# Kernel optimization log

Hardware: AMD Instinct MI355X
Metric: run time of the kernel (lower is better)

## Reference

```python
import jax, jax.numpy as jnp
import numpy as np

D_MODEL = 512
N_HEAD = 8


def setup_inputs() -> dict:
    key = jax.random.key(0)
    ks = jax.random.split(key, 9)
    s = 1.0 / np.sqrt(D_MODEL)
    inp = {
        "x": jax.random.normal(ks[0], (2, 4096, D_MODEL), dtype=jnp.float32),
        "wq": jax.random.uniform(ks[1], (D_MODEL, D_MODEL), jnp.float32, -s, s),
        "bq": jax.random.uniform(ks[2], (D_MODEL,), jnp.float32, -s, s),
        "wk": jax.random.uniform(ks[3], (D_MODEL, D_MODEL), jnp.float32, -s, s),
        "bk": jax.random.uniform(ks[4], (D_MODEL,), jnp.float32, -s, s),
        "wv": jax.random.uniform(ks[5], (D_MODEL, D_MODEL), jnp.float32, -s, s),
        "bv": jax.random.uniform(ks[6], (D_MODEL,), jnp.float32, -s, s),
        "wo": jax.random.uniform(ks[7], (D_MODEL, D_MODEL), jnp.float32, -s, s),
        "bo": jax.random.uniform(ks[8], (D_MODEL,), jnp.float32, -s, s),
    }
    return inp


def reference(x, wq, bq, wk, bk, wv, bv, wo, bo):
    B, S, D = x.shape
    H = N_HEAD
    Dh = D // H

    def split_heads(t):  # [B,S,D] -> [B,H,S,Dh]
        return t.reshape(B, S, H, Dh).transpose(0, 2, 1, 3)

    q = split_heads(x @ wq.T + bq)
    k = split_heads(x @ wk.T + bk)
    v = split_heads(x @ wv.T + bv)

    # explicit (unfused) attention, matching the torch module
    score = jnp.einsum("bhsd,bhtd->bhst", q, k) / jnp.sqrt(jnp.float32(Dh))
    attn = jax.nn.softmax(score, axis=-1)
    out = jnp.einsum("bhst,bhtd->bhsd", attn, v)  # [B,H,S,Dh]

    out = out.transpose(0, 2, 1, 3).reshape(B, S, D)
    return out @ wo.T + bo
```

## Files before the change

### kernel.cpp

```cpp
#include <hip/hip_runtime.h>
#include <math.h>

#define S_LEN 4096
#define DMODEL 512
#define NHEAD 8
#define E_ELEMS ((size_t)8192 * 512)
#define QSCALE 0.18033688f

typedef __attribute__((ext_vector_type(8))) short bf16x8;
typedef __attribute__((ext_vector_type(4))) float f32x4;
typedef __attribute__((ext_vector_type(16))) float f32x16;
typedef unsigned short u16;
typedef unsigned int u32;

__device__ __forceinline__ u16 f2bf(float f) {
    u32 u = __float_as_uint(f);
    u += 0x7FFFu + ((u >> 16) & 1u);
    return (u16)(u >> 16);
}
__device__ __forceinline__ float bf2f(u16 h) {
    return __uint_as_float((u32)h << 16);
}

#define MFMA16(a, b, c) __builtin_amdgcn_mfma_f32_16x16x32_bf16((a), (b), (c), 0, 0, 0)
#define MFMA32(a, b, c) __builtin_amdgcn_mfma_f32_32x32x16_bf16((a), (b), (c), 0, 0, 0)

__global__ __launch_bounds__(256) void cvt_all(
    const float* __restrict__ x,
    const float* __restrict__ wq, const float* __restrict__ wk,
    const float* __restrict__ wv, const float* __restrict__ wo,
    u16* __restrict__ xbf, u16* __restrict__ oq, u16* __restrict__ ok,
    u16* __restrict__ ov, u16* __restrict__ oo)
{
    const int bid = blockIdx.x;
    if (bid < 4096) {
        const int i = bid * 256 + threadIdx.x;
        const float4 v = ((const float4*)x)[i];
        uint2 hp;
        hp.x = (u32)f2bf(v.x) | ((u32)f2bf(v.y) << 16);
        hp.y = (u32)f2bf(v.z) | ((u32)f2bf(v.w) << 16);
        ((uint2*)xbf)[i] = hp;
    } else {
        const int i = (bid - 4096) * 256 + threadIdx.x;
        {
            const float4 v = ((const float4*)wq)[i];
            uint2 hp;
            hp.x = (u32)f2bf(v.x * QSCALE) | ((u32)f2bf(v.y * QSCALE) << 16);
            hp.y = (u32)f2bf(v.z * QSCALE) | ((u32)f2bf(v.w * QSCALE) << 16);
            ((uint2*)oq)[i] = hp;
        }
        {
            const float4 v = ((const float4*)wk)[i];
            uint2 hp;
            hp.x = (u32)f2bf(v.x) | ((u32)f2bf(v.y) << 16);
            hp.y = (u32)f2bf(v.z) | ((u32)f2bf(v.w) << 16);
            ((uint2*)ok)[i] = hp;
        }
        {
            const float4 v = ((const float4*)wv)[i];
            uint2 hp;
            hp.x = (u32)f2bf(v.x) | ((u32)f2bf(v.y) << 16);
            hp.y = (u32)f2bf(v.z) | ((u32)f2bf(v.w) << 16);
            ((uint2*)ov)[i] = hp;
        }
        {
            const float4 v = ((const float4*)wo)[i];
            uint2 hp;
            hp.x = (u32)f2bf(v.x) | ((u32)f2bf(v.y) << 16);
            hp.y = (u32)f2bf(v.z) | ((u32)f2bf(v.w) << 16);
            ((uint2*)oo)[i] = hp;
        }
    }
}

template<int MODE>
__global__ __launch_bounds__(256) void proj2_kernel(
    const u16* __restrict__ Abf,
    const u16* __restrict__ W0, const float* __restrict__ Bi0,
    const u16* __restrict__ W1, const float* __restrict__ Bi1,
    const u16* __restrict__ W2, const float* __restrict__ Bi2,
    u16* __restrict__ Qo, u16* __restrict__ Ko, u16* __restrict__ Vt,
    float* __restrict__ Out)
{
    __shared__ __align__(16) u16 sm[18432];
    u16* As = sm;
    u16* Bs = sm + 8192;

    const int tid = threadIdx.x;
    const int w = tid >> 6, l = tid & 63, g = (l >> 4), c = l & 15;
    const int wr = w >> 1, wc = w & 1;
    const int bm = blockIdx.x * 128;
    const int n0 = blockIdx.y * 128;
    const int z = (MODE == 0) ? blockIdx.z : 0;
    const u16* W   = (z == 0) ? W0 : (z == 1) ? W1 : W2;
    const float* Bi = (z == 0) ? Bi0 : (z == 1) ? Bi1 : Bi2;
    const float bsc = (MODE == 0 && z == 0) ? QSCALE : 1.0f;

    const int sr = l >> 3;
    const int slot = l & 7;

    f32x4 acc[4][4];
    #pragma unroll
    for (int i = 0; i < 4; ++i)
        #pragma unroll
        for (int j = 0; j < 4; ++j) acc[i][j] = (f32x4){0.f, 0.f, 0.f, 0.f};

    #pragma unroll 1
    for (int kt = 0; kt < 8; ++kt) {
        const int k0 = kt * 64;
        __syncthreads();
        #pragma unroll
        for (int i = 0; i < 4; ++i) {
            const int row = i * 32 + w * 8 + sr;
            const int scol = (slot ^ (row & 7)) * 8;
            __builtin_amdgcn_global_load_lds(
                Abf + (size_t)(bm + row) * DMODEL + k0 + scol,
                As + (i * 32 + w * 8) * 64, 16, 0, 0);
            __builtin_amdgcn_global_load_lds(
                W + (size_t)(n0 + row) * DMODEL + k0 + scol,
                Bs + (i * 32 + w * 8) * 64, 16, 0, 0);
        }
        __syncthreads();

        #pragma unroll
        for (int kc = 0; kc < 2; ++kc) {
            bf16x8 a[4], b[4];
            #pragma unroll
            for (int mf = 0; mf < 4; ++mf) {
                const int ra = wr * 64 + mf * 16 + c;
                a[mf] = *(const bf16x8*)(As + ra * 64 + (((kc * 4 + g) ^ (ra & 7)) * 8));
            }
            #pragma unroll
            for (int nf = 0; nf < 4; ++nf) {
                const int rb = wc * 64 + nf * 16 + c;
                b[nf] = *(const bf16x8*)(Bs + rb * 64 + (((kc * 4 + g) ^ (rb & 7)) * 8));
            }
            #pragma unroll
            for (int mf = 0; mf < 4; ++mf)
                #pragma unroll
                for (int nf = 0; nf < 4; ++nf)
                    acc[mf][nf] = MFMA16(a[mf], b[nf], acc[mf][nf]);
        }
    }

    if (MODE == 0 && z == 2) {
        __syncthreads();
        float* scr = (float*)sm;
        const int d = tid & 63, sb = tid >> 6;
        const int b = bm >> 12;
        #pragma unroll
        for (int pass = 0; pass < 2; ++pass) {
            if (wc == pass) {
                #pragma unroll
                for (int mf = 0; mf < 4; ++mf)
                    #pragma unroll
                    for (int nf = 0; nf < 4; ++nf) {
                        const float bias = Bi[n0 + pass * 64 + nf * 16 + c];
                        #pragma unroll
                        for (int r = 0; r < 4; ++r)
                            scr[(wr * 64 + mf * 16 + 4 * g + r) * 72 + nf * 16 + c] =
                                acc[mf][nf][r] + bias;
                    }
            }
            __syncthreads();
            const int hh = (n0 >> 6) + pass;
            const size_t obase =
                ((size_t)((b * NHEAD + hh) * 64 + d)) * S_LEN + (bm & (S_LEN - 1)) + sb * 32;
            u16 th[32];
            #pragma unroll
            for (int j = 0; j < 32; ++j)
                th[j] = f2bf(scr[(sb * 32 + j) * 72 + d]);
            #pragma unroll
            for (int q4 = 0; q4 < 4; ++q4)
                *(uint4*)(Vt + obase + q4 * 8) = *(const uint4*)&th[q4 * 8];
            __syncthreads();
        }
        return;
    }

    #pragma unroll
    for (int mf = 0; mf < 4; ++mf)
        #pragma unroll
        for (int nf = 0; nf < 4; ++nf) {
            const int n = n0 + wc * 64 + nf * 16 + c;
            const float bias = Bi[n] * bsc;
            #pragma unroll
            for (int r = 0; r < 4; ++r) {
                const int m = bm + wr * 64 + mf * 16 + 4 * g + r;
                const float v = acc[mf][nf][r] + bias;
                if (MODE == 1) {
                    Out[(size_t)m * DMODEL + n] = v;
                } else {
                    const int b = m >> 12, s = m & (S_LEN - 1);
                    const int hh = n >> 6, dd = n & 63;
                    const size_t o = ((size_t)((b * NHEAD + hh) * S_LEN + s)) * 64 + dd;
                    if (z == 0) Qo[o] = f2bf(v);
                    else        Ko[o] = f2bf(v);
                }
            }
        }
}

__global__ __launch_bounds__(256, 2) void attn_kernel(
    const u16* __restrict__ Qb, const u16* __restrict__ Kb,
    const u16* __restrict__ Vt, u16* __restrict__ OpB, float* __restrict__ Lp)
{
    __shared__ __align__(16) u16 sm[24576];

    const int tid = threadIdx.x;
    const int w = tid >> 6, l = tid & 63;
    const int r0 = l & 31, hi = l >> 5;

    const int f = blockIdx.x;
    const int wg = (f & 7) * 64 + (f >> 3);
    const int bh = wg >> 5, kvh = (wg >> 4) & 1, qb = wg & 15;
    const int b = bh >> 3, h = bh & 7;

    const size_t hoff = (size_t)bh * S_LEN * 64;
    const int qw = qb * 256 + w * 64;
    const int kv0 = kvh * 2048;

    bf16x8 qf[2][4];
    #pragma unroll
    for (int qfi = 0; qfi < 2; ++qfi)
        #pragma unroll
        for (int kc = 0; kc < 4; ++kc)
            qf[qfi][kc] = *(const bf16x8*)(Qb + hoff +
                (size_t)(qw + qfi * 32 + r0) * 64 + kc * 16 + hi * 8);

    const int rbase = r0 * 64;
    int soff[4];
    #pragma unroll
    for (int j = 0; j < 4; ++j) soff[j] = ((2 * j + hi) ^ (r0 & 7)) * 8;

    const int srow0 = w * 16 + (l >> 3);
    const int slot  = l & 7;
    const int srow1 = srow0 + 8;
    const u16* srcK0 = Kb + hoff + (size_t)(kv0 + srow0) * 64 + ((slot ^ (srow0 & 7)) * 8);
    const u16* srcK1 = Kb + hoff + (size_t)(kv0 + srow1) * 64 + ((slot ^ (srow1 & 7)) * 8);
    const u16* srcV0 = Vt + ((size_t)bh * 64 + srow0) * S_LEN + kv0 + ((slot ^ (srow0 & 7)) * 8);
    const u16* srcV1 = Vt + ((size_t)bh * 64 + srow1) * S_LEN + kv0 + ((slot ^ (srow1 & 7)) * 8);

#define STAGE(bufb, t) do {                                                        \
        u16* kb_ = sm + (bufb) * 8192 + w * 1024;                                  \
        u16* vb_ = kb_ + 4096;                                                     \
        __builtin_amdgcn_global_load_lds(srcK0 + (size_t)(t) * 4096, kb_,       16, 0, 0); \
        __builtin_amdgcn_global_load_lds(srcK1 + (size_t)(t) * 4096, kb_ + 512, 16, 0, 0); \
        __builtin_amdgcn_global_load_lds(srcV0 + (size_t)(t) * 64,   vb_,       16, 0, 0); \
        __builtin_amdgcn_global_load_lds(srcV1 + (size_t)(t) * 64,   vb_ + 512, 16, 0, 0); \
    } while (0)

#define ZERO16 {0.f,0.f,0.f,0.f,0.f,0.f,0.f,0.f,0.f,0.f,0.f,0.f,0.f,0.f,0.f,0.f}
    f32x16 o00 = ZERO16, o01 = ZERO16, o10 = ZERO16, o11 = ZERO16;
    float lA = 0.f, lB = 0.f;

    auto compute_tile = [&](const u16* Kb_s, const u16* Vb_s) {
        #pragma unroll
        for (int kvf = 0; kvf < 2; ++kvf) {
            f32x16 sA = ZERO16, sB = ZERO16;
            __builtin_amdgcn_s_setprio(1);
            #pragma unroll
            for (int kc = 0; kc < 4; ++kc) {
                const bf16x8 k = *(const bf16x8*)(Kb_s + kvf * 2048 + rbase + soff[kc]);
                sA = MFMA32(k, qf[0][kc], sA);
                sB = MFMA32(k, qf[1][kc], sB);
            }
            __builtin_amdgcn_s_setprio(0);

            #pragma unroll
            for (int r = 0; r < 16; ++r) {
                sA[r] = __builtin_amdgcn_exp2f(sA[r]);
                sB[r] = __builtin_amdgcn_exp2f(sB[r]);
            }
            #pragma unroll
            for (int r = 0; r < 16; ++r) { lA += sA[r]; lB += sB[r]; }

            #pragma unroll
            for (int hf = 0; hf < 2; ++hf) {
                const int rb = hf * 8;
                const int idx = kvf * 2 + hf;
                u32 x0, y0, x1, y1;
                asm("v_cvt_pk_bf16_f32 %0, %1, %2" : "=v"(x0) : "v"(sA[rb+0]), "v"(sA[rb+1]));
                asm("v_cvt_pk_bf16_f32 %0, %1, %2" : "=v"(y0) : "v"(sA[rb+4]), "v"(sA[rb+5]));
                asm("v_cvt_pk_bf16_f32 %0, %1, %2" : "=v"(x1) : "v"(sA[rb+2]), "v"(sA[rb+3]));
                asm("v_cvt_pk_bf16_f32 %0, %1, %2" : "=v"(y1) : "v"(sA[rb+6]), "v"(sA[rb+7]));
                asm volatile("v_permlane32_swap_b32 %0, %1" : "+v"(x0), "+v"(y0));
                asm volatile("v_permlane32_swap_b32 %0, %1" : "+v"(x1), "+v"(y1));
                union { u32 u[4]; bf16x8 v; } PA;
                PA.u[0] = x0; PA.u[1] = x1; PA.u[2] = y0; PA.u[3] = y1;
                asm("v_cvt_pk_bf16_f32 %0, %1, %2" : "=v"(x0) : "v"(sB[rb+0]), "v"(sB[rb+1]));
                asm("v_cvt_pk_bf16_f32 %0, %1, %2" : "=v"(y0) : "v"(sB[rb+4]), "v"(sB[rb+5]));
                asm("v_cvt_pk_bf16_f32 %0, %1, %2" : "=v"(x1) : "v"(sB[rb+2]), "v"(sB[rb+3]));
                asm("v_cvt_pk_bf16_f32 %0, %1, %2" : "=v"(y1) : "v"(sB[rb+6]), "v"(sB[rb+7]));
                asm volatile("v_permlane32_swap_b32 %0, %1" : "+v"(x0), "+v"(y0));
                asm volatile("v_permlane32_swap_b32 %0, %1" : "+v"(x1), "+v"(y1));
                union { u32 u[4]; bf16x8 v; } PB;
                PB.u[0] = x0; PB.u[1] = x1; PB.u[2] = y0; PB.u[3] = y1;

                const bf16x8 v0 = *(const bf16x8*)(Vb_s + rbase + soff[idx]);
                const bf16x8 v1 = *(const bf16x8*)(Vb_s + 2048 + rbase + soff[idx]);
                __builtin_amdgcn_s_setprio(1);
                o00 = MFMA32(PA.v, v0, o00);
                o01 = MFMA32(PA.v, v1, o01);
                o10 = MFMA32(PB.v, v0, o10);
                o11 = MFMA32(PB.v, v1, o11);
                __builtin_amdgcn_s_setprio(0);
            }
        }
    };

    STAGE(0, 0);
    STAGE(1, 1);

    #pragma unroll 1
    for (int t = 0; t < 31; ++t) {
        asm volatile("s_waitcnt vmcnt(4)" ::: "memory");
        __builtin_amdgcn_s_barrier();
        __builtin_amdgcn_sched_barrier(0);
        if (t < 30) STAGE((t + 2) % 3, t + 2);
        const u16* Kb_s = sm + (t % 3) * 8192;
        compute_tile(Kb_s, Kb_s + 4096);
    }
    {
        asm volatile("s_waitcnt vmcnt(0)" ::: "memory");
        __builtin_amdgcn_s_barrier();
        __builtin_amdgcn_sched_barrier(0);
        const u16* Kb_s = sm + (31 % 3) * 8192;
        compute_tile(Kb_s, Kb_s + 4096);
    }
#undef STAGE

    lA += __shfl_xor(lA, 32);
    lB += __shfl_xor(lB, 32);
    if (hi == 0) {
        Lp[((size_t)kvh * 16 + bh) * S_LEN + qw + r0]      = lA;
        Lp[((size_t)kvh * 16 + bh) * S_LEN + qw + 32 + r0] = lB;
    }

    u16* Ob = OpB + (size_t)kvh * E_ELEMS + (size_t)b * S_LEN * DMODEL;
    #pragma unroll
    for (int qfi = 0; qfi < 2; ++qfi)
        #pragma unroll
        for (int df = 0; df < 2; ++df) {
            #pragma unroll
            for (int r = 0; r < 16; ++r) {
                const float ov = qfi ? (df ? o11[r] : o10[r]) : (df ? o01[r] : o00[r]);
                const int q = qfi * 32 + (r & 3) + 8 * (r >> 2) + 4 * hi;
                Ob[(size_t)(qw + q) * DMODEL + h * 64 + df * 32 + r0] = f2bf(ov);
            }
        }
}

__global__ __launch_bounds__(256) void combine_kernel(
    const u16* __restrict__ Op, const float* __restrict__ Lp,
    u16* __restrict__ A)
{
    const int i = blockIdx.x * 256 + threadIdx.x;
    const int m = i >> 6;
    const int col = (i & 63) * 8;
    const int b = m >> 12, s = m & (S_LEN - 1), h = col >> 6;
    const int bh = b * 8 + h;

    const float lt = Lp[(size_t)bh * S_LEN + s] +
                     Lp[((size_t)16 + bh) * S_LEN + s];
    const float inv = 1.0f / lt;

    float acc[8] = {};
    #pragma unroll
    for (int kq = 0; kq < 2; ++kq) {
        const uint4 v = *(const uint4*)(Op + (size_t)kq * E_ELEMS + (size_t)m * DMODEL + col);
        const u16* p = (const u16*)&v;
        #pragma unroll
        for (int j = 0; j < 8; ++j) acc[j] += bf2f(p[j]);
    }
    u16 r[8];
    #pragma unroll
    for (int j = 0; j < 8; ++j) r[j] = f2bf(acc[j] * inv);
    *(uint4*)(A + (size_t)m * DMODEL + col) = *(const uint4*)r;
}

extern "C" void kernel_launch(void* const* d_in, const int* in_sizes, int n_in,
                              void* d_out, int out_size, void* d_ws, size_t ws_size,
                              hipStream_t stream)
{
    const float* x  = (const float*)d_in[0];
    const float* wq = (const float*)d_in[1];
    const float* bq = (const float*)d_in[2];
    const float* wk = (const float*)d_in[3];
    const float* bk = (const float*)d_in[4];
    const float* wv = (const float*)d_in[5];
    const float* bv = (const float*)d_in[6];
    const float* wo = (const float*)d_in[7];
    const float* bo = (const float*)d_in[8];

    u16* ws = (u16*)d_ws;
    const size_t E = E_ELEMS;
    u16* xbf  = ws;
    u16* Qbf  = ws + E;
    u16* Kbf  = ws + 2 * E;
    u16* Vtbf = ws + 3 * E;
    u16* wqbf = ws + 4 * E;
    u16* wkbf = wqbf + DMODEL * DMODEL;
    u16* wvbf = wkbf + DMODEL * DMODEL;
    u16* wobf = wvbf + DMODEL * DMODEL;
    u16* OpB  = wobf + DMODEL * DMODEL;
    float* Lp = (float*)(OpB + 2 * E);

    cvt_all<<<dim3(4352), 256, 0, stream>>>(
        x, wq, wk, wv, wo, xbf, wqbf, wkbf, wvbf, wobf);

    proj2_kernel<0><<<dim3(64, 4, 3), 256, 0, stream>>>(
        xbf, wqbf, bq, wkbf, bk, wvbf, bv, Qbf, Kbf, Vtbf, nullptr);

    attn_kernel<<<dim3(512), 256, 0, stream>>>(Qbf, Kbf, Vtbf, OpB, Lp);

    combine_kernel<<<dim3(2048), 256, 0, stream>>>(OpB, Lp, xbf);

    proj2_kernel<1><<<dim3(64, 4, 1), 256, 0, stream>>>(
        xbf, wobf, bo, nullptr, nullptr, nullptr, nullptr,
        nullptr, nullptr, nullptr, (float*)d_out);
}
```

Before: 126.5 us.

## Split attention KV into three chunks and fuse combine via last-block counter

The attention grid grows from 512 to 768 workgroups by splitting the KV range into three uneven chunks instead of two. This is meant to fill the 256 CUs more evenly with two blocks per CU. The separate combine kernel is removed: an atomic per-(head, query-block) counter lets the last-finishing block sum the three bf16 partials and normalise them. Costs include a third partial buffer, extra memory traffic, threadfence and atomic overhead, and a combine tail that runs only in the last blocks.

```diff
diff --git a/kernel.cpp b/kernel.cpp
--- a/kernel.cpp
+++ b/kernel.cpp
@@ -30,9 +30,13 @@
     const float* __restrict__ wq, const float* __restrict__ wk,
     const float* __restrict__ wv, const float* __restrict__ wo,
     u16* __restrict__ xbf, u16* __restrict__ oq, u16* __restrict__ ok,
-    u16* __restrict__ ov, u16* __restrict__ oo)
+    u16* __restrict__ ov, u16* __restrict__ oo, u32* __restrict__ cnt)
 {
     const int bid = blockIdx.x;
+    if (bid >= 4352) {
+        if (threadIdx.x < 256) cnt[threadIdx.x] = 0;
+        return;
+    }
     if (bid < 4096) {
         const int i = bid * 256 + threadIdx.x;
         const float4 v = ((const float4*)x)[i];
@@ -203,22 +207,28 @@
 
 __global__ __launch_bounds__(256, 2) void attn_kernel(
     const u16* __restrict__ Qb, const u16* __restrict__ Kb,
-    const u16* __restrict__ Vt, u16* __restrict__ OpB, float* __restrict__ Lp)
+    const u16* __restrict__ Vt, u16* __restrict__ OpB, float* __restrict__ Lp,
+    u32* __restrict__ cnt, u16* __restrict__ AO)
 {
     __shared__ __align__(16) u16 sm[24576];
+    __shared__ u32 lastflag;
 
     const int tid = threadIdx.x;
     const int w = tid >> 6, l = tid & 63;
     const int r0 = l & 31, hi = l >> 5;
 
     const int f = blockIdx.x;
-    const int wg = (f & 7) * 64 + (f >> 3);
-    const int bh = wg >> 5, kvh = (wg >> 4) & 1, qb = wg & 15;
+    const int wg = (f & 7) * 96 + (f >> 3);
+    const int bh = wg / 48;
+    const int rem = wg - bh * 48;
+    const int kvs = rem >> 4, qb = rem & 15;
     const int b = bh >> 3, h = bh & 7;
 
     const size_t hoff = (size_t)bh * S_LEN * 64;
     const int qw = qb * 256 + w * 64;
-    const int kv0 = kvh * 2048;
+    const int t0 = (kvs * 64) / 3;
+    const int NT = ((kvs + 1) * 64) / 3 - t0;
+    const int kv0 = t0 * 64;
 
     bf16x8 qf[2][4];
     #pragma unroll
@@ -313,11 +323,11 @@
     STAGE(1, 1);
 
     #pragma unroll 1
-    for (int t = 0; t < 31; ++t) {
+    for (int t = 0; t < NT - 1; ++t) {
         asm volatile("s_waitcnt vmcnt(4)" ::: "memory");
         __builtin_amdgcn_s_barrier();
         __builtin_amdgcn_sched_barrier(0);
-        if (t < 30) STAGE((t + 2) % 3, t + 2);
+        if (t < NT - 2) STAGE((t + 2) % 3, t + 2);
         const u16* Kb_s = sm + (t % 3) * 8192;
         compute_tile(Kb_s, Kb_s + 4096);
     }
@@ -325,7 +335,7 @@
         asm volatile("s_waitcnt vmcnt(0)" ::: "memory");
         __builtin_amdgcn_s_barrier();
         __builtin_amdgcn_sched_barrier(0);
-        const u16* Kb_s = sm + (31 % 3) * 8192;
+        const u16* Kb_s = sm + ((NT - 1) % 3) * 8192;
         compute_tile(Kb_s, Kb_s + 4096);
     }
 #undef STAGE
@@ -333,11 +343,11 @@
     lA += __shfl_xor(lA, 32);
     lB += __shfl_xor(lB, 32);
     if (hi == 0) {
-        Lp[((size_t)kvh * 16 + bh) * S_LEN + qw + r0]      = lA;
-        Lp[((size_t)kvh * 16 + bh) * S_LEN + qw + 32 + r0] = lB;
-    }
-
-    u16* Ob = OpB + (size_t)kvh * E_ELEMS + (size_t)b * S_LEN * DMODEL;
+        Lp[((size_t)kvs * 16 + bh) * S_LEN + qw + r0]      = lA;
+        Lp[((size_t)kvs * 16 + bh) * S_LEN + qw + 32 + r0] = lB;
+    }
+
+    u16* Ob = OpB + (size_t)kvs * E_ELEMS + (size_t)b * S_LEN * DMODEL;
     #pragma unroll
     for (int qfi = 0; qfi < 2; ++qfi)
         #pragma unroll
@@ -349,34 +359,38 @@
                 Ob[(size_t)(qw + q) * DMODEL + h * 64 + df * 32 + r0] = f2bf(ov);
             }
         }
-}
-
-__global__ __launch_bounds__(256) void combine_kernel(
-    const u16* __restrict__ Op, const float* __restrict__ Lp,
-    u16* __restrict__ A)
-{
-    const int i = blockIdx.x * 256 + threadIdx.x;
-    const int m = i >> 6;
-    const int col = (i & 63) * 8;
-    const int b = m >> 12, s = m & (S_LEN - 1), h = col >> 6;
-    const int bh = b * 8 + h;
-
-    const float lt = Lp[(size_t)bh * S_LEN + s] +
-                     Lp[((size_t)16 + bh) * S_LEN + s];
-    const float inv = 1.0f / lt;
-
-    float acc[8] = {};
-    #pragma unroll
-    for (int kq = 0; kq < 2; ++kq) {
-        const uint4 v = *(const uint4*)(Op + (size_t)kq * E_ELEMS + (size_t)m * DMODEL + col);
-        const u16* p = (const u16*)&v;
-        #pragma unroll
-        for (int j = 0; j < 8; ++j) acc[j] += bf2f(p[j]);
-    }
-    u16 r[8];
-    #pragma unroll
-    for (int j = 0; j < 8; ++j) r[j] = f2bf(acc[j] * inv);
-    *(uint4*)(A + (size_t)m * DMODEL + col) = *(const uint4*)r;
+
+    __threadfence();
+    if (tid == 0) lastflag = atomicAdd(&cnt[bh * 16 + qb], 1u);
+    __syncthreads();
+    if (lastflag != 2u) return;
+    __threadfence();
+
+    const float* L0 = Lp + (size_t)bh * S_LEN;
+    const float* L1 = Lp + ((size_t)16 + bh) * S_LEN;
+    const float* L2 = Lp + ((size_t)32 + bh) * S_LEN;
+    #pragma unroll 1
+    for (int it = 0; it < 8; ++it) {
+        const int e = it * 2048 + tid * 8;
+        const int j = e >> 6;
+        const int colc = e & 63;
+        const int s = qb * 256 + j;
+        const float lt = L0[s] + L1[s] + L2[s];
+        const float inv = 1.0f / lt;
+        const size_t a = ((size_t)(b * S_LEN + s)) * DMODEL + h * 64 + colc;
+        float acc[8] = {};
+        #pragma unroll
+        for (int kq = 0; kq < 3; ++kq) {
+            const uint4 v = *(const uint4*)(OpB + (size_t)kq * E_ELEMS + a);
+            const u16* p = (const u16*)&v;
+            #pragma unroll
+            for (int jj = 0; jj < 8; ++jj) acc[jj] += bf2f(p[jj]);
+        }
+        u16 rr[8];
+        #pragma unroll
+        for (int jj = 0; jj < 8; ++jj) rr[jj] = f2bf(acc[jj] * inv);
+        *(uint4*)(AO + a) = *(const uint4*)rr;
+    }
 }
 
 extern "C" void kernel_launch(void* const* d_in, const int* in_sizes, int n_in,
@@ -404,17 +418,16 @@
     u16* wvbf = wkbf + DMODEL * DMODEL;
     u16* wobf = wvbf + DMODEL * DMODEL;
     u16* OpB  = wobf + DMODEL * DMODEL;
-    float* Lp = (float*)(OpB + 2 * E);
-
-    cvt_all<<<dim3(4352), 256, 0, stream>>>(
-        x, wq, wk, wv, wo, xbf, wqbf, wkbf, wvbf, wobf);
+    float* Lp = (float*)(OpB + 3 * E);
+    u32* cnt  = (u32*)(Lp + (size_t)3 * 16 * S_LEN);
+
+    cvt_all<<<dim3(4353), 256, 0, stream>>>(
+        x, wq, wk, wv, wo, xbf, wqbf, wkbf, wvbf, wobf, cnt);
 
     proj2_kernel<0><<<dim3(64, 4, 3), 256, 0, stream>>>(
         xbf, wqbf, bq, wkbf, bk, wvbf, bv, Qbf, Kbf, Vtbf, nullptr);
 
-    attn_kernel<<<dim3(512), 256, 0, stream>>>(Qbf, Kbf, Vtbf, OpB, Lp);
-
-    combine_kernel<<<dim3(2048), 256, 0, stream>>>(OpB, Lp, xbf);
+    attn_kernel<<<dim3(768), 256, 0, stream>>>(Qbf, Kbf, Vtbf, OpB, Lp, cnt, xbf);
 
     proj2_kernel<1><<<dim3(64, 4, 1), 256, 0, stream>>>(
         xbf, wobf, bo, nullptr, nullptr, nullptr, nullptr,
```

New measurement: 226.5 us. 79.0% more time.
